# Performance work log

Hardware: AMD Instinct MI355X
Metric: run time of the kernel (lower is better)

The kernel has to match this reference:

```python
import jax, jax.numpy as jnp
import numpy as np

DIM = 768
HEADS = 8
EPS = 1e-6


def _layernorm(x, gamma, beta):
    # torch: mean over last dim; std with Bessel correction (unbiased, ddof=1)
    mean = jnp.mean(x, axis=-1, keepdims=True)
    std = jnp.std(x, axis=-1, keepdims=True, ddof=1)
    return gamma * (x - mean) / (std + EPS) + beta


def setup_inputs() -> dict:
    key = jax.random.key(0)
    ks = jax.random.split(key, 8)
    s = 0.02
    return {
        "x": jax.random.normal(ks[0], (16384, DIM), dtype=jnp.float32),
        "wq_w": jax.random.normal(ks[1], (DIM, DIM), dtype=jnp.float32) * s,
        "wq_b": jnp.zeros((DIM,), dtype=jnp.float32),
        "wk_w": jax.random.normal(ks[2], (DIM, DIM), dtype=jnp.float32) * s,
        "wk_b": jnp.zeros((DIM,), dtype=jnp.float32),
        "wv_w": jax.random.normal(ks[3], (DIM, DIM), dtype=jnp.float32) * s,
        "wv_b": jnp.zeros((DIM,), dtype=jnp.float32),
        "d1_w": jax.random.normal(ks[4], (4 * DIM, DIM), dtype=jnp.float32) * s,
        "d1_b": jnp.zeros((4 * DIM,), dtype=jnp.float32),
        "d2_w": jax.random.normal(ks[5], (DIM, 4 * DIM), dtype=jnp.float32) * s,
        "d2_b": jnp.zeros((DIM,), dtype=jnp.float32),
        "g1": jnp.ones((1,), dtype=jnp.float32),
        "b1": jnp.zeros((1,), dtype=jnp.float32),
        "g2": jnp.ones((1,), dtype=jnp.float32),
        "b2": jnp.zeros((1,), dtype=jnp.float32),
    }


def reference(x, wq_w, wq_b, wk_w, wk_b, wv_w, wv_b,
              d1_w, d1_b, d2_w, d2_b, g1, b1, g2, b2):
    T = x.shape[0]
    # --- pre-LN + attention ---
    xn = _layernorm(x, g1, b1)                      # [T, D]
    q = xn @ wq_w.T + wq_b                          # [T, D]
    k = xn @ wk_w.T + wk_b
    v = xn @ wv_w.T + wv_b
    # faithful to q.view(-1, num_heads, key_dim): groups of HEADS tokens
    q = q.reshape(T // HEADS, HEADS, DIM)
    k = k.reshape(T // HEADS, HEADS, DIM)
    v = v.reshape(T // HEADS, HEADS, DIM)
    scores = jnp.einsum('ghd,gkd->ghk', q, k) / jnp.sqrt(jnp.float32(DIM))
    attn_w = jax.nn.softmax(scores, axis=-1)        # [T/8, 8, 8]
    attn = jnp.einsum('ghk,gkd->ghd', attn_w, v).reshape(T, DIM)
    x = attn + x
    # --- pre-LN + MLP ---
    xn = _layernorm(x, g2, b2)
    h = jax.nn.gelu(xn @ d1_w.T + d1_b, approximate=False)  # [T, 4D]
    x = (h @ d2_w.T + d2_b) + x
    return x
```

## Files before the change

kernel.cpp:

```cpp
#include <hip/hip_runtime.h>
#include <stdint.h>

#define DIM 768
#define HDIM 3072

typedef unsigned short u16;
typedef unsigned char u8;
typedef __bf16 bf16x8 __attribute__((ext_vector_type(8)));
typedef __bf16 bf16x4 __attribute__((ext_vector_type(4)));
typedef float f32x4 __attribute__((ext_vector_type(4)));
typedef float f32x16 __attribute__((ext_vector_type(16)));
typedef int i32x8 __attribute__((ext_vector_type(8)));

__device__ __forceinline__ float b2f(u16 u) {
    union { unsigned i; float f; } v; v.i = ((unsigned)u) << 16; return v.f;
}
__device__ __forceinline__ u16 f2b(float f) {
    union { float f; unsigned i; } v; v.f = f;
    unsigned r = (v.i + 0x7FFFu + ((v.i >> 16) & 1u)) >> 16;
    return (u16)r;
}
__device__ __forceinline__ unsigned pack2b(float a, float b) {
    return (unsigned)f2b(a) | ((unsigned)f2b(b) << 16);
}
__device__ __forceinline__ float gelu_f(float v) {
    float u = v * (1.5957691216f + 0.07135481627f * v * v);
    float e = __builtin_amdgcn_exp2f(-1.442695041f * u);
    return v * __builtin_amdgcn_rcpf(1.0f + e);
}
__device__ __forceinline__ void gl_lds16(const void* g, void* l) {
    __builtin_amdgcn_global_load_lds(
        (__attribute__((address_space(1))) void*)(g),
        (__attribute__((address_space(3))) void*)(l), 16, 0, 0);
}

__global__ __launch_bounds__(256) void cvt_bf16(const float4* __restrict__ s,
                                                ushort4* __restrict__ d, int n4) {
    int i = blockIdx.x * 256 + threadIdx.x;
    if (i < n4) {
        float4 v = s[i];
        ushort4 o;
        o.x = f2b(v.x); o.y = f2b(v.y); o.z = f2b(v.z); o.w = f2b(v.w);
        d[i] = o;
    }
}

__global__ __launch_bounds__(256) void cvt_fp8(const float4* __restrict__ s,
                                               unsigned* __restrict__ d, int n4) {
    int i = blockIdx.x * 256 + threadIdx.x;
    if (i < n4) {
        float4 v = s[i];
        int p = __builtin_amdgcn_cvt_pk_fp8_f32(v.x, v.y, 0, false);
        p = __builtin_amdgcn_cvt_pk_fp8_f32(v.z, v.w, p, true);
        d[i] = (unsigned)p;
    }
}

__global__ void pack_bias3(const float* __restrict__ a, const float* __restrict__ b,
                           const float* __restrict__ c, float* __restrict__ o) {
    int i = blockIdx.x * 256 + threadIdx.x;
    if (i < DIM) { o[i] = a[i]; o[i + DIM] = b[i]; o[i + 2 * DIM] = c[i]; }
}

__global__ __launch_bounds__(256) void ln_rows_f8(const float* __restrict__ x, u8* __restrict__ xn,
                                                  const float* __restrict__ g, const float* __restrict__ b) {
    int row = blockIdx.x * 4 + (threadIdx.x >> 6);
    int lane = threadIdx.x & 63;
    const float* xr = x + (size_t)row * DIM + lane * 12;
    float v[12];
#pragma unroll
    for (int i = 0; i < 3; ++i) {
        float4 t = ((const float4*)xr)[i];
        v[i * 4 + 0] = t.x; v[i * 4 + 1] = t.y; v[i * 4 + 2] = t.z; v[i * 4 + 3] = t.w;
    }
    float s = 0.f, ss = 0.f;
#pragma unroll
    for (int i = 0; i < 12; ++i) { s += v[i]; ss += v[i] * v[i]; }
#pragma unroll
    for (int o = 32; o; o >>= 1) { s += __shfl_xor(s, o); ss += __shfl_xor(ss, o); }
    float mean = s * (1.f / DIM);
    float var = (ss - (float)DIM * mean * mean) * (1.f / (DIM - 1));
    float denom = sqrtf(var) + 1e-6f;
    float sc = g[0] / denom, bb = b[0] - mean * sc;
    unsigned* outp = (unsigned*)(xn + (size_t)row * DIM + lane * 12);
#pragma unroll
    for (int i = 0; i < 3; ++i) {
        int p = __builtin_amdgcn_cvt_pk_fp8_f32(v[i * 4 + 0] * sc + bb, v[i * 4 + 1] * sc + bb, 0, false);
        p = __builtin_amdgcn_cvt_pk_fp8_f32(v[i * 4 + 2] * sc + bb, v[i * 4 + 3] * sc + bb, p, true);
        outp[i] = (unsigned)p;
    }
}

template <int EPI, int N, int K>
__global__ __launch_bounds__(256)
void gemm_f8(const u8* __restrict__ A, const u8* __restrict__ B,
             const float* __restrict__ bias, const float* __restrict__ resid,
             u16* __restrict__ Cb, float* __restrict__ Cf) {
    __shared__ __align__(16) u8 As[128 * 128];
    __shared__ __align__(16) u8 Bs[128 * 128];
    const int tid = threadIdx.x, lane = tid & 63, wave = tid >> 6;
    const int row0 = blockIdx.x * 128, col0 = blockIdx.y * 128;
    const int wm = (wave >> 1) * 64, wn = (wave & 1) * 64;
    f32x16 acc[2][2] = {};

    const int srow = lane >> 3;
    const int schunk = ((lane & 7) ^ srow) * 16;
    const u8* Ag = A + (size_t)(row0 + wave * 8 + srow) * K + schunk;
    const u8* Bg = B + (size_t)(col0 + wave * 8 + srow) * K + schunk;
    const size_t s32 = (size_t)32 * K;
    u8* AsW = As + wave * 1024;
    u8* BsW = Bs + wave * 1024;

    const int r31 = lane & 31, khalf = lane >> 5;

    for (int kb = 0; kb < K; kb += 128) {
#pragma unroll
        for (int i = 0; i < 4; ++i) {
            gl_lds16(Ag + i * s32, AsW + i * 4096);
            gl_lds16(Bg + i * s32, BsW + i * 4096);
        }
        Ag += 128; Bg += 128;
        __syncthreads();
#pragma unroll
        for (int ks = 0; ks < 2; ++ks) {
            const int c0 = ks * 4 + khalf * 2;
            union { i32x8 v; uint4 q[2]; } af[2], bfr[2];
#pragma unroll
            for (int ib = 0; ib < 2; ++ib) {
                const int r = wm + ib * 32 + r31;
                const u8* base = As + r * 128;
                const int x7 = (r & 7);
                af[ib].q[0] = *(const uint4*)(base + ((c0 ^ x7) * 16));
                af[ib].q[1] = *(const uint4*)(base + (((c0 + 1) ^ x7) * 16));
            }
#pragma unroll
            for (int jb = 0; jb < 2; ++jb) {
                const int r = wn + jb * 32 + r31;
                const u8* base = Bs + r * 128;
                const int x7 = (r & 7);
                bfr[jb].q[0] = *(const uint4*)(base + ((c0 ^ x7) * 16));
                bfr[jb].q[1] = *(const uint4*)(base + (((c0 + 1) ^ x7) * 16));
            }
#pragma unroll
            for (int ib = 0; ib < 2; ++ib)
#pragma unroll
                for (int jb = 0; jb < 2; ++jb)
                    acc[ib][jb] = __builtin_amdgcn_mfma_scale_f32_32x32x64_f8f6f4(
                        bfr[jb].v, af[ib].v, acc[ib][jb], 0, 0,
                        0, 0x7F7F7F7F, 0, 0x7F7F7F7F);
        }
        __syncthreads();
    }
#pragma unroll
    for (int ib = 0; ib < 2; ++ib) {
        const int row = row0 + wm + ib * 32 + r31;
#pragma unroll
        for (int jb = 0; jb < 2; ++jb) {
#pragma unroll
            for (int gq = 0; gq < 4; ++gq) {
                const int cb = col0 + wn + jb * 32 + gq * 8 + 4 * khalf;
                float4 bv = *(const float4*)(bias + cb);
                float v0 = acc[ib][jb][gq * 4 + 0] + bv.x;
                float v1 = acc[ib][jb][gq * 4 + 1] + bv.y;
                float v2 = acc[ib][jb][gq * 4 + 2] + bv.z;
                float v3 = acc[ib][jb][gq * 4 + 3] + bv.w;
                const size_t idx = (size_t)row * N + cb;
                if (EPI == 2) {
                    float4 rv = *(const float4*)(resid + idx);
                    float4 o; o.x = v0 + rv.x; o.y = v1 + rv.y; o.z = v2 + rv.z; o.w = v3 + rv.w;
                    *(float4*)(Cf + idx) = o;
                } else {
                    uint2 o; o.x = pack2b(v0, v1); o.y = pack2b(v2, v3);
                    *(uint2*)(Cb + idx) = o;
                }
            }
        }
    }
}

template <int N, int K>
__global__ __launch_bounds__(256)
void gemm_up(const u16* __restrict__ A, const u16* __restrict__ B,
             const float* __restrict__ bias, u8* __restrict__ C8) {
    __shared__ __align__(16) u16 As[128 * 64];
    __shared__ __align__(16) u16 Bs[128 * 64];
    const int tid = threadIdx.x;
    const int row0 = blockIdx.x * 128, col0 = blockIdx.y * 128;
    const int lane = tid & 63, wave = tid >> 6;
    const int wm = (wave >> 1) * 64, wn = (wave & 1) * 64;
    const int la = lane & 15, qd = lane >> 4;
    f32x4 acc[4][4] = {};

    const int srow = lane >> 3;
    const int schunk = (lane & 7) ^ srow;
    const u16* Ag = A + (size_t)(row0 + wave * 8 + srow) * K + schunk * 8;
    const u16* Bg = B + (size_t)(col0 + wave * 8 + srow) * K + schunk * 8;
    const size_t s32 = (size_t)32 * K;
    u16* AsW = &As[wave * 512];
    u16* BsW = &Bs[wave * 512];
    const int x7 = la & 7;

    for (int kb = 0; kb < K; kb += 64) {
#pragma unroll
        for (int i = 0; i < 4; ++i) {
            gl_lds16(Ag + i * s32, AsW + i * 2048);
            gl_lds16(Bg + i * s32, BsW + i * 2048);
        }
        Ag += 64; Bg += 64;
        __syncthreads();
#pragma unroll
        for (int ks = 0; ks < 2; ++ks) {
            const int cp = ((ks * 4 + qd) ^ x7) * 8;
            bf16x8 af[4], bfr[4];
#pragma unroll
            for (int i = 0; i < 4; ++i)
                af[i] = *(const bf16x8*)(&As[(wm + i * 16 + la) * 64 + cp]);
#pragma unroll
            for (int j = 0; j < 4; ++j)
                bfr[j] = *(const bf16x8*)(&Bs[(wn + j * 16 + la) * 64 + cp]);
#pragma unroll
            for (int i = 0; i < 4; ++i)
#pragma unroll
                for (int j = 0; j < 4; ++j)
                    acc[i][j] = __builtin_amdgcn_mfma_f32_16x16x32_bf16(bfr[j], af[i], acc[i][j], 0, 0, 0);
        }
        __syncthreads();
    }
#pragma unroll
    for (int i = 0; i < 4; ++i) {
        const int row = row0 + wm + i * 16 + la;
#pragma unroll
        for (int j = 0; j < 4; ++j) {
            const int cb = col0 + wn + j * 16 + qd * 4;
            float4 bv = *(const float4*)(bias + cb);
            float v0 = gelu_f(acc[i][j][0] + bv.x);
            float v1 = gelu_f(acc[i][j][1] + bv.y);
            float v2 = gelu_f(acc[i][j][2] + bv.z);
            float v3 = gelu_f(acc[i][j][3] + bv.w);
            int p = __builtin_amdgcn_cvt_pk_fp8_f32(v0, v1, 0, false);
            p = __builtin_amdgcn_cvt_pk_fp8_f32(v2, v3, p, true);
            *(unsigned*)(C8 + (size_t)row * N + cb) = (unsigned)p;
        }
    }
}

__global__ __launch_bounds__(256)
void attn_ln(const u16* __restrict__ qkv, const float* __restrict__ x,
             float* __restrict__ x1, u16* __restrict__ xn2,
             const float* __restrict__ g, const float* __restrict__ b) {
    __shared__ __align__(16) u16 sq[8 * 2304];
    __shared__ float sw[64];
    const int tid = threadIdx.x;
    const size_t gbase = (size_t)blockIdx.x * (8 * 2304);
    const uint4* src = (const uint4*)(qkv + gbase);
    uint4* dst = (uint4*)sq;
#pragma unroll
    for (int i = 0; i < 9; ++i) dst[tid + i * 256] = src[tid + i * 256];
    __syncthreads();
    const int wave = tid >> 6, lane = tid & 63;
#pragma unroll 2
    for (int p = wave * 16; p < wave * 16 + 16; ++p) {
        const u16* qr = sq + (p >> 3) * 2304;
        const u16* kr = sq + (p & 7) * 2304 + 768;
        bf16x8 qa = *(const bf16x8*)(qr + lane * 8);
        bf16x8 ka = *(const bf16x8*)(kr + lane * 8);
        bf16x4 qb = *(const bf16x4*)(qr + 512 + lane * 4);
        bf16x4 kb = *(const bf16x4*)(kr + 512 + lane * 4);
        float s = 0.f;
#pragma unroll
        for (int i = 0; i < 8; ++i) s += (float)qa[i] * (float)ka[i];
#pragma unroll
        for (int i = 0; i < 4; ++i) s += (float)qb[i] * (float)kb[i];
#pragma unroll
        for (int o = 32; o; o >>= 1) s += __shfl_xor(s, o);
        if (lane == 0) sw[p] = s;
    }
    __syncthreads();
    if (tid < 8) {
        const float scl = 0.03608439182435161f;
        float e[8]; float m = -1e30f;
#pragma unroll
        for (int j = 0; j < 8; ++j) m = fmaxf(m, sw[tid * 8 + j]);
        float sum = 0.f;
#pragma unroll
        for (int j = 0; j < 8; ++j) { e[j] = expf((sw[tid * 8 + j] - m) * scl); sum += e[j]; }
        float inv = 1.f / sum;
#pragma unroll
        for (int j = 0; j < 8; ++j) sw[tid * 8 + j] = e[j] * inv;
    }
    __syncthreads();
    const int h = tid >> 5, li = tid & 31;
    float w[8];
#pragma unroll
    for (int kk = 0; kk < 8; ++kk) w[kk] = sw[h * 8 + kk];
    const size_t trow = (size_t)blockIdx.x * 8 + h;
    const float* xr = x + trow * DIM;
    float* x1r = x1 + trow * DIM;
    float xv[24], s = 0.f, ss = 0.f;
#pragma unroll
    for (int wd = 0; wd < 3; ++wd) {
        const int d0 = wd * 256 + li * 8;
        float o[8] = {};
#pragma unroll
        for (int kk = 0; kk < 8; ++kk) {
            bf16x8 vv = *(const bf16x8*)(sq + kk * 2304 + 1536 + d0);
#pragma unroll
            for (int e = 0; e < 8; ++e) o[e] += w[kk] * (float)vv[e];
        }
        float4 xa = *(const float4*)(xr + d0);
        float4 xb = *(const float4*)(xr + d0 + 4);
        float vals[8] = { o[0] + xa.x, o[1] + xa.y, o[2] + xa.z, o[3] + xa.w,
                          o[4] + xb.x, o[5] + xb.y, o[6] + xb.z, o[7] + xb.w };
        float4 w0, w1;
        w0.x = vals[0]; w0.y = vals[1]; w0.z = vals[2]; w0.w = vals[3];
        w1.x = vals[4]; w1.y = vals[5]; w1.z = vals[6]; w1.w = vals[7];
        *(float4*)(x1r + d0) = w0;
        *(float4*)(x1r + d0 + 4) = w1;
#pragma unroll
        for (int e = 0; e < 8; ++e) {
            xv[wd * 8 + e] = vals[e];
            s += vals[e]; ss += vals[e] * vals[e];
        }
    }
#pragma unroll
    for (int o2 = 16; o2; o2 >>= 1) { s += __shfl_xor(s, o2); ss += __shfl_xor(ss, o2); }
    float mean = s * (1.f / 768.f);
    float var = (ss - 768.f * mean * mean) * (1.f / 767.f);
    float denom = sqrtf(var) + 1e-6f;
    float sc = g[0] / denom, bb = b[0] - mean * sc;
    u16* xnr = xn2 + trow * DIM;
#pragma unroll
    for (int wd = 0; wd < 3; ++wd) {
        const int d0 = wd * 256 + li * 8;
        uint4 o;
        o.x = pack2b(xv[wd * 8 + 0] * sc + bb, xv[wd * 8 + 1] * sc + bb);
        o.y = pack2b(xv[wd * 8 + 2] * sc + bb, xv[wd * 8 + 3] * sc + bb);
        o.z = pack2b(xv[wd * 8 + 4] * sc + bb, xv[wd * 8 + 5] * sc + bb);
        o.w = pack2b(xv[wd * 8 + 6] * sc + bb, xv[wd * 8 + 7] * sc + bb);
        *(uint4*)(xnr + d0) = o;
    }
}

extern "C" void kernel_launch(void* const* d_in, const int* in_sizes, int n_in,
                              void* d_out, int out_size, void* d_ws, size_t ws_size,
                              hipStream_t stream) {
    (void)n_in; (void)out_size; (void)ws_size;
    const float* x    = (const float*)d_in[0];
    const float* wq_w = (const float*)d_in[1];
    const float* wq_b = (const float*)d_in[2];
    const float* wk_w = (const float*)d_in[3];
    const float* wk_b = (const float*)d_in[4];
    const float* wv_w = (const float*)d_in[5];
    const float* wv_b = (const float*)d_in[6];
    const float* d1_w = (const float*)d_in[7];
    const float* d1_b = (const float*)d_in[8];
    const float* d2_w = (const float*)d_in[9];
    const float* d2_b = (const float*)d_in[10];
    const float* g1 = (const float*)d_in[11];
    const float* b1 = (const float*)d_in[12];
    const float* g2 = (const float*)d_in[13];
    const float* b2 = (const float*)d_in[14];
    float* out = (float*)d_out;
    char* ws = (char*)d_ws;

    const int T = in_sizes[0] / DIM;

    u8*    w_qkv8 = (u8*)(ws);
    u16*   w_d1   = (u16*)(ws + 1769472);
    u8*    w_d28  = (u8*)(ws + 6488064);
    float* b_qkv  = (float*)(ws + 8847360);
    u16*   xn2    = (u16*)(ws + 8856576);
    float* x1     = (float*)(ws + 34022400);
    u8*    xn1_8  = (u8*)(ws + 34022400);
    u16*   qkv    = (u16*)(ws + 84354048);
    u8*    h8     = (u8*)(ws + 84354048);

    cvt_fp8<<<576, 256, 0, stream>>>((const float4*)wq_w, (unsigned*)w_qkv8, 147456);
    cvt_fp8<<<576, 256, 0, stream>>>((const float4*)wk_w, (unsigned*)(w_qkv8 + 589824), 147456);
    cvt_fp8<<<576, 256, 0, stream>>>((const float4*)wv_w, (unsigned*)(w_qkv8 + 1179648), 147456);
    cvt_bf16<<<2304, 256, 0, stream>>>((const float4*)d1_w, (ushort4*)w_d1, 589824);
    cvt_fp8<<<2304, 256, 0, stream>>>((const float4*)d2_w, (unsigned*)w_d28, 589824);
    pack_bias3<<<3, 256, 0, stream>>>(wq_b, wk_b, wv_b, b_qkv);

    ln_rows_f8<<<T / 4, 256, 0, stream>>>(x, xn1_8, g1, b1);
    gemm_f8<0, 2304, 768><<<dim3(T / 128, 18), 256, 0, stream>>>(xn1_8, w_qkv8, b_qkv, nullptr, qkv, nullptr);
    attn_ln<<<T / 8, 256, 0, stream>>>(qkv, x, x1, xn2, g2, b2);
    gemm_up<3072, 768><<<dim3(T / 128, 24), 256, 0, stream>>>(xn2, w_d1, d1_b, h8);
    gemm_f8<2, 768, 3072><<<dim3(T / 128, 6), 256, 0, stream>>>(h8, w_d28, d2_b, x1, nullptr, out);
}
```

Measured before the change: 416.7 us.

## Store QKV in fp8 and stage GEMM epilogues through LDS for coalesced stores

The QKV projection now writes fp8 instead of bf16, which halves that intermediate's write and read traffic, and the attention kernel decodes fp8 with packed conversion instructions. All three GEMM epilogues (QKV, up-projection, down-projection with residual) now go through swizzled shared memory, so each thread writes full 16-byte rows contiguously instead of small scattered stores. Storing q, k and v in fp8 lowers attention precision, and the staging adds LDS traffic and extra barriers.

```diff
diff --git a/kernel.cpp b/kernel.cpp
--- a/kernel.cpp
+++ b/kernel.cpp
@@ -6,15 +6,13 @@
 
 typedef unsigned short u16;
 typedef unsigned char u8;
+typedef unsigned int u32;
 typedef __bf16 bf16x8 __attribute__((ext_vector_type(8)));
-typedef __bf16 bf16x4 __attribute__((ext_vector_type(4)));
+typedef float f32x2 __attribute__((ext_vector_type(2)));
 typedef float f32x4 __attribute__((ext_vector_type(4)));
 typedef float f32x16 __attribute__((ext_vector_type(16)));
 typedef int i32x8 __attribute__((ext_vector_type(8)));
 
-__device__ __forceinline__ float b2f(u16 u) {
-    union { unsigned i; float f; } v; v.i = ((unsigned)u) << 16; return v.f;
-}
 __device__ __forceinline__ u16 f2b(float f) {
     union { float f; unsigned i; } v; v.f = f;
     unsigned r = (v.i + 0x7FFFu + ((v.i >> 16) & 1u)) >> 16;
@@ -95,9 +93,10 @@
 __global__ __launch_bounds__(256)
 void gemm_f8(const u8* __restrict__ A, const u8* __restrict__ B,
              const float* __restrict__ bias, const float* __restrict__ resid,
-             u16* __restrict__ Cb, float* __restrict__ Cf) {
-    __shared__ __align__(16) u8 As[128 * 128];
-    __shared__ __align__(16) u8 Bs[128 * 128];
+             u8* __restrict__ Co, float* __restrict__ Cf) {
+    __shared__ __align__(16) u8 smem[32768];
+    u8* As = smem;
+    u8* Bs = smem + 16384;
     const int tid = threadIdx.x, lane = tid & 63, wave = tid >> 6;
     const int row0 = blockIdx.x * 128, col0 = blockIdx.y * 128;
     const int wm = (wave >> 1) * 64, wn = (wave & 1) * 64;
@@ -151,29 +150,72 @@
         }
         __syncthreads();
     }
-#pragma unroll
-    for (int ib = 0; ib < 2; ++ib) {
-        const int row = row0 + wm + ib * 32 + r31;
-#pragma unroll
-        for (int jb = 0; jb < 2; ++jb) {
-#pragma unroll
-            for (int gq = 0; gq < 4; ++gq) {
-                const int cb = col0 + wn + jb * 32 + gq * 8 + 4 * khalf;
-                float4 bv = *(const float4*)(bias + cb);
-                float v0 = acc[ib][jb][gq * 4 + 0] + bv.x;
-                float v1 = acc[ib][jb][gq * 4 + 1] + bv.y;
-                float v2 = acc[ib][jb][gq * 4 + 2] + bv.z;
-                float v3 = acc[ib][jb][gq * 4 + 3] + bv.w;
-                const size_t idx = (size_t)row * N + cb;
-                if (EPI == 2) {
-                    float4 rv = *(const float4*)(resid + idx);
-                    float4 o; o.x = v0 + rv.x; o.y = v1 + rv.y; o.z = v2 + rv.z; o.w = v3 + rv.w;
-                    *(float4*)(Cf + idx) = o;
-                } else {
-                    uint2 o; o.x = pack2b(v0, v1); o.y = pack2b(v2, v3);
-                    *(uint2*)(Cb + idx) = o;
+    if (EPI == 0) {
+        u32* Cs = (u32*)smem;
+#pragma unroll
+        for (int ib = 0; ib < 2; ++ib) {
+            const int row = wm + ib * 32 + r31;
+            const int rx = row & 31;
+#pragma unroll
+            for (int jb = 0; jb < 2; ++jb)
+#pragma unroll
+                for (int gq = 0; gq < 4; ++gq) {
+                    const int cb = wn + jb * 32 + gq * 8 + 4 * khalf;
+                    float4 bv = *(const float4*)(bias + col0 + cb);
+                    float v0 = acc[ib][jb][gq * 4 + 0] + bv.x;
+                    float v1 = acc[ib][jb][gq * 4 + 1] + bv.y;
+                    float v2 = acc[ib][jb][gq * 4 + 2] + bv.z;
+                    float v3 = acc[ib][jb][gq * 4 + 3] + bv.w;
+                    int p = __builtin_amdgcn_cvt_pk_fp8_f32(v0, v1, 0, false);
+                    p = __builtin_amdgcn_cvt_pk_fp8_f32(v2, v3, p, true);
+                    Cs[row * 32 + ((cb >> 2) ^ rx)] = (u32)p;
                 }
+        }
+        __syncthreads();
+#pragma unroll
+        for (int pr = 0; pr < 4; ++pr) {
+            const int r = pr * 32 + (tid >> 3);
+            const int rx = r & 31;
+            const int dwb = (tid & 7) * 4;
+            uint4 o;
+            o.x = Cs[r * 32 + ((dwb + 0) ^ rx)];
+            o.y = Cs[r * 32 + ((dwb + 1) ^ rx)];
+            o.z = Cs[r * 32 + ((dwb + 2) ^ rx)];
+            o.w = Cs[r * 32 + ((dwb + 3) ^ rx)];
+            *(uint4*)(Co + (size_t)(row0 + r) * N + col0 + dwb * 4) = o;
+        }
+    } else {
+        float* Cs = (float*)smem;
+#pragma unroll
+        for (int pass = 0; pass < 2; ++pass) {
+            const int ss = (wm >> 1) + r31;
+            const int sx = ss & 7;
+#pragma unroll
+            for (int jb = 0; jb < 2; ++jb)
+#pragma unroll
+                for (int gq = 0; gq < 4; ++gq) {
+                    const int cb = wn + jb * 32 + gq * 8 + 4 * khalf;
+                    float4 bv = *(const float4*)(bias + col0 + cb);
+                    float4 v;
+                    v.x = acc[pass][jb][gq * 4 + 0] + bv.x;
+                    v.y = acc[pass][jb][gq * 4 + 1] + bv.y;
+                    v.z = acc[pass][jb][gq * 4 + 2] + bv.z;
+                    v.w = acc[pass][jb][gq * 4 + 3] + bv.w;
+                    *(float4*)(Cs + ss * 128 + (((cb >> 2) ^ sx) << 2)) = v;
+                }
+            __syncthreads();
+            const int s = tid >> 2;
+            const int grow = row0 + (s >> 5) * 64 + pass * 32 + (s & 31);
+#pragma unroll
+            for (int k = 0; k < 8; ++k) {
+                const int c = k * 4 + (tid & 3);
+                float4 v = *(const float4*)(Cs + s * 128 + ((c ^ (s & 7)) << 2));
+                const size_t gi = (size_t)grow * N + col0 + c * 4;
+                float4 rv = *(const float4*)(resid + gi);
+                v.x += rv.x; v.y += rv.y; v.z += rv.z; v.w += rv.w;
+                *(float4*)(Cf + gi) = v;
             }
+            if (pass == 0) __syncthreads();
         }
     }
 }
@@ -226,51 +268,70 @@
         }
         __syncthreads();
     }
+    u32* Cs = (u32*)As;
 #pragma unroll
     for (int i = 0; i < 4; ++i) {
-        const int row = row0 + wm + i * 16 + la;
+        const int row = wm + i * 16 + la;
+        const int rx = row & 31;
 #pragma unroll
         for (int j = 0; j < 4; ++j) {
-            const int cb = col0 + wn + j * 16 + qd * 4;
-            float4 bv = *(const float4*)(bias + cb);
+            const int cb = wn + j * 16 + qd * 4;
+            float4 bv = *(const float4*)(bias + col0 + cb);
             float v0 = gelu_f(acc[i][j][0] + bv.x);
             float v1 = gelu_f(acc[i][j][1] + bv.y);
             float v2 = gelu_f(acc[i][j][2] + bv.z);
             float v3 = gelu_f(acc[i][j][3] + bv.w);
             int p = __builtin_amdgcn_cvt_pk_fp8_f32(v0, v1, 0, false);
             p = __builtin_amdgcn_cvt_pk_fp8_f32(v2, v3, p, true);
-            *(unsigned*)(C8 + (size_t)row * N + cb) = (unsigned)p;
-        }
+            Cs[row * 32 + ((cb >> 2) ^ rx)] = (u32)p;
+        }
+    }
+    __syncthreads();
+#pragma unroll
+    for (int pr = 0; pr < 4; ++pr) {
+        const int r = pr * 32 + (tid >> 3);
+        const int rx = r & 31;
+        const int dwb = (tid & 7) * 4;
+        uint4 o;
+        o.x = Cs[r * 32 + ((dwb + 0) ^ rx)];
+        o.y = Cs[r * 32 + ((dwb + 1) ^ rx)];
+        o.z = Cs[r * 32 + ((dwb + 2) ^ rx)];
+        o.w = Cs[r * 32 + ((dwb + 3) ^ rx)];
+        *(uint4*)(C8 + (size_t)(row0 + r) * N + col0 + dwb * 4) = o;
     }
 }
 
 __global__ __launch_bounds__(256)
-void attn_ln(const u16* __restrict__ qkv, const float* __restrict__ x,
+void attn_ln(const u8* __restrict__ qkv, const float* __restrict__ x,
              float* __restrict__ x1, u16* __restrict__ xn2,
              const float* __restrict__ g, const float* __restrict__ b) {
-    __shared__ __align__(16) u16 sq[8 * 2304];
+    __shared__ __align__(16) u8 sq[8 * 2304];
     __shared__ float sw[64];
     const int tid = threadIdx.x;
-    const size_t gbase = (size_t)blockIdx.x * (8 * 2304);
-    const uint4* src = (const uint4*)(qkv + gbase);
+    const uint4* src = (const uint4*)(qkv + (size_t)blockIdx.x * (8 * 2304));
     uint4* dst = (uint4*)sq;
 #pragma unroll
-    for (int i = 0; i < 9; ++i) dst[tid + i * 256] = src[tid + i * 256];
+    for (int i = 0; i < 5; ++i) {
+        int idx = tid + i * 256;
+        if (idx < 1152) dst[idx] = src[idx];
+    }
     __syncthreads();
+    const u32* sq32 = (const u32*)sq;
     const int wave = tid >> 6, lane = tid & 63;
 #pragma unroll 2
     for (int p = wave * 16; p < wave * 16 + 16; ++p) {
-        const u16* qr = sq + (p >> 3) * 2304;
-        const u16* kr = sq + (p & 7) * 2304 + 768;
-        bf16x8 qa = *(const bf16x8*)(qr + lane * 8);
-        bf16x8 ka = *(const bf16x8*)(kr + lane * 8);
-        bf16x4 qb = *(const bf16x4*)(qr + 512 + lane * 4);
-        bf16x4 kb = *(const bf16x4*)(kr + 512 + lane * 4);
+        const u32* qr = sq32 + (p >> 3) * 576 + lane * 3;
+        const u32* kr = sq32 + (p & 7) * 576 + 192 + lane * 3;
         float s = 0.f;
 #pragma unroll
-        for (int i = 0; i < 8; ++i) s += (float)qa[i] * (float)ka[i];
-#pragma unroll
-        for (int i = 0; i < 4; ++i) s += (float)qb[i] * (float)kb[i];
+        for (int i = 0; i < 3; ++i) {
+            u32 qd = qr[i], kd = kr[i];
+            f32x2 q0 = __builtin_amdgcn_cvt_pk_f32_fp8(qd, false);
+            f32x2 q1 = __builtin_amdgcn_cvt_pk_f32_fp8(qd, true);
+            f32x2 k0 = __builtin_amdgcn_cvt_pk_f32_fp8(kd, false);
+            f32x2 k1 = __builtin_amdgcn_cvt_pk_f32_fp8(kd, true);
+            s += q0[0] * k0[0] + q0[1] * k0[1] + q1[0] * k1[0] + q1[1] * k1[1];
+        }
 #pragma unroll
         for (int o = 32; o; o >>= 1) s += __shfl_xor(s, o);
         if (lane == 0) sw[p] = s;
@@ -303,9 +364,15 @@
         float o[8] = {};
 #pragma unroll
         for (int kk = 0; kk < 8; ++kk) {
-            bf16x8 vv = *(const bf16x8*)(sq + kk * 2304 + 1536 + d0);
-#pragma unroll
-            for (int e = 0; e < 8; ++e) o[e] += w[kk] * (float)vv[e];
+            uint2 vv = *(const uint2*)(sq32 + kk * 576 + 384 + wd * 64 + li * 2);
+            f32x2 a0 = __builtin_amdgcn_cvt_pk_f32_fp8(vv.x, false);
+            f32x2 a1 = __builtin_amdgcn_cvt_pk_f32_fp8(vv.x, true);
+            f32x2 a2 = __builtin_amdgcn_cvt_pk_f32_fp8(vv.y, false);
+            f32x2 a3 = __builtin_amdgcn_cvt_pk_f32_fp8(vv.y, true);
+            o[0] += w[kk] * a0[0]; o[1] += w[kk] * a0[1];
+            o[2] += w[kk] * a1[0]; o[3] += w[kk] * a1[1];
+            o[4] += w[kk] * a2[0]; o[5] += w[kk] * a2[1];
+            o[6] += w[kk] * a3[0]; o[7] += w[kk] * a3[1];
         }
         float4 xa = *(const float4*)(xr + d0);
         float4 xb = *(const float4*)(xr + d0 + 4);
@@ -372,7 +439,7 @@
     u16*   xn2    = (u16*)(ws + 8856576);
     float* x1     = (float*)(ws + 34022400);
     u8*    xn1_8  = (u8*)(ws + 34022400);
-    u16*   qkv    = (u16*)(ws + 84354048);
+    u8*    qkv8   = (u8*)(ws + 84354048);
     u8*    h8     = (u8*)(ws + 84354048);
 
     cvt_fp8<<<576, 256, 0, stream>>>((const float4*)wq_w, (unsigned*)w_qkv8, 147456);
@@ -383,8 +450,8 @@
     pack_bias3<<<3, 256, 0, stream>>>(wq_b, wk_b, wv_b, b_qkv);
 
     ln_rows_f8<<<T / 4, 256, 0, stream>>>(x, xn1_8, g1, b1);
-    gemm_f8<0, 2304, 768><<<dim3(T / 128, 18), 256, 0, stream>>>(xn1_8, w_qkv8, b_qkv, nullptr, qkv, nullptr);
-    attn_ln<<<T / 8, 256, 0, stream>>>(qkv, x, x1, xn2, g2, b2);
+    gemm_f8<0, 2304, 768><<<dim3(T / 128, 18), 256, 0, stream>>>(xn1_8, w_qkv8, b_qkv, nullptr, qkv8, nullptr);
+    attn_ln<<<T / 8, 256, 0, stream>>>(qkv8, x, x1, xn2, g2, b2);
     gemm_up<3072, 768><<<dim3(T / 128, 24), 256, 0, stream>>>(xn2, w_d1, d1_b, h8);
     gemm_f8<2, 768, 3072><<<dim3(T / 128, 6), 256, 0, stream>>>(h8, w_d28, d2_b, x1, nullptr, out);
 }
```

Result: faster. 369.4 us (-11.3%).
